# Optimization experiments

Hardware: AMD Instinct MI355X
Metric: run time of the kernel (lower is better)

The kernel has to match this reference:

```python
import jax, jax.numpy as jnp
import numpy as np

B, S, DIM = 1, 2048, 4096
NH, NKV, HD = 32, 8, 128
REPEATS = NH // NKV
ROPE_THETA = 10000.0


def setup_inputs() -> dict:
    key = jax.random.key(0)
    ks = jax.random.split(key, 6)
    x = jax.random.normal(ks[0], (B, S, DIM), jnp.float32) * 0.02
    wq = jax.random.normal(ks[1], (NH * HD, DIM), jnp.float32) * 0.02
    wk = jax.random.normal(ks[2], (NKV * HD, DIM), jnp.float32) * 0.02
    wv = jax.random.normal(ks[3], (NKV * HD, DIM), jnp.float32) * 0.02
    wo = jax.random.normal(ks[4], (DIM, NH * HD), jnp.float32) * 0.02
    # rotary frequencies (real cos/sin form of complex freqs_cis)
    inv_freq = 1.0 / (ROPE_THETA ** (jnp.arange(0, HD, 2, dtype=jnp.float32) / HD))
    ang = jnp.arange(S, dtype=jnp.float32)[:, None] * inv_freq[None, :]  # [S, HD//2]
    freqs_cos = jnp.cos(ang)
    freqs_sin = jnp.sin(ang)
    positions = jnp.arange(S, dtype=jnp.int32)  # prompt phase: all positions
    # additive causal mask
    mask = jnp.where(jnp.tril(jnp.ones((S, S), bool)), 0.0, -1e9).astype(jnp.float32)
    cache_k = jnp.zeros((B, S, NKV, HD), jnp.float32)
    cache_v = jnp.zeros((B, S, NKV, HD), jnp.float32)
    return dict(x=x, wq=wq, wk=wk, wv=wv, wo=wo, freqs_cos=freqs_cos,
                freqs_sin=freqs_sin, cache_k=cache_k, cache_v=cache_v,
                positions=positions, mask=mask)


def apply_rope(t, cos, sin):
    # t: [b, s, h, d]; pairs are (d0,d1),(d2,d3),... matching view_as_complex
    tr = t[..., 0::2]
    ti = t[..., 1::2]
    c = cos[None, :, None, :]
    s = sin[None, :, None, :]
    out_r = tr * c - ti * s
    out_i = tr * s + ti * c
    return jnp.stack([out_r, out_i], axis=-1).reshape(t.shape)


def reference(x, wq, wk, wv, wo, freqs_cos, freqs_sin, cache_k, cache_v, positions, mask):
    b, s, _ = x.shape
    xq = jnp.einsum('bsd,od->bso', x, wq).reshape(b, s, NH, HD)
    xk = jnp.einsum('bsd,od->bso', x, wk).reshape(b, s, NKV, HD)
    xv = jnp.einsum('bsd,od->bso', x, wv).reshape(b, s, NKV, HD)
    xq = apply_rope(xq, freqs_cos, freqs_sin)
    xk = apply_rope(xk, freqs_cos, freqs_sin)
    # KV-cache scatter (prompt phase writes; output uses fresh xk/xv here)
    cache_k = cache_k.at[:, positions].set(xk)
    cache_v = cache_v.at[:, positions].set(xv)
    # GQA: repeat_interleave kv heads to match query heads
    k = jnp.repeat(xk, REPEATS, axis=2).transpose(0, 2, 1, 3)  # [b, NH, s, HD]
    v = jnp.repeat(xv, REPEATS, axis=2).transpose(0, 2, 1, 3)
    q = xq.transpose(0, 2, 1, 3)
    scale = HD ** -0.5
    scores = jnp.einsum('bhqd,bhkd->bhqk', q, k) * scale + mask[None, None]
    probs = jax.nn.softmax(scores.astype(jnp.float32), axis=-1).astype(q.dtype)
    out = jnp.einsum('bhqk,bhkd->bhqd', probs, v)
    out = out.transpose(0, 2, 1, 3).reshape(b, s, NH * HD)
    return jnp.einsum('bso,do->bsd', out, wo)
```

## Files before the change

### kernel.cpp

```cpp
#include <hip/hip_runtime.h>
#include <hip/hip_bf16.h>
#include <stdint.h>

typedef __bf16 bf16_t;
typedef __attribute__((ext_vector_type(8))) __bf16 bf16x8;
typedef __attribute__((ext_vector_type(4))) float f32x4;
typedef __attribute__((ext_vector_type(8))) unsigned short u16x8;

#define S_LEN 2048
#define DIM   4096
#define QKVN  6144
#define NHEAD 32
#define HDIM  128

typedef __attribute__((address_space(1))) unsigned int as1_u32;
typedef __attribute__((address_space(3))) unsigned int as3_u32;

__device__ __forceinline__ unsigned short f2bf(float f) {
  unsigned u = __builtin_bit_cast(unsigned, f);
  u += 0x7fffu + ((u >> 16) & 1u);
  return (unsigned short)(u >> 16);
}

__device__ __forceinline__ void gload_lds16(const void* g, void* l) {
  __builtin_amdgcn_global_load_lds(
      (as1_u32*)(unsigned long long)(uintptr_t)g,
      (as3_u32*)(unsigned int)(uintptr_t)l,
      16, 0, 0);
}

__global__ __launch_bounds__(256) void cvt5_kernel(const float* __restrict__ x,
                                                   const float* __restrict__ wq,
                                                   const float* __restrict__ wk,
                                                   const float* __restrict__ wv,
                                                   const float* __restrict__ wo,
                                                   ushort4* __restrict__ xb,
                                                   ushort4* __restrict__ wqkvb,
                                                   ushort4* __restrict__ wob) {
  const long N0 = 2097152;
  const long N1 = N0 + 4194304;
  const long N2 = N1 + 1048576;
  const long N3 = N2 + 1048576;
  const long N4 = N3 + 4194304;
  long idx = (long)blockIdx.x * 256 + threadIdx.x;
  long stride = (long)gridDim.x * 256;
  for (long i = idx; i < N4; i += stride) {
    const float4* s; ushort4* d; long o;
    if (i < N0)      { s = (const float4*)x;  d = xb;              o = i; }
    else if (i < N1) { s = (const float4*)wq; d = wqkvb;           o = i - N0; }
    else if (i < N2) { s = (const float4*)wk; d = wqkvb + 4194304; o = i - N1; }
    else if (i < N3) { s = (const float4*)wv; d = wqkvb + 5242880; o = i - N2; }
    else             { s = (const float4*)wo; d = wob;             o = i - N3; }
    float4 v = s[o];
    ushort4 r;
    r.x = f2bf(v.x); r.y = f2bf(v.y); r.z = f2bf(v.z); r.w = f2bf(v.w);
    d[o] = r;
  }
}

__device__ __forceinline__ bf16x8 fld(const char* half, int row, int chunk) {
  return *(const bf16x8*)(half + row * 128 + ((chunk ^ (row & 7)) << 4));
}

template <int OUTF32>
__global__ __launch_bounds__(512, 2) void gemm8q(const bf16_t* __restrict__ A,
                                                 const bf16_t* __restrict__ B,
                                                 void* __restrict__ Cout,
                                                 int M, int N, int K, int nxt) {
  __shared__ char lds[147456];
  const int tid = threadIdx.x;
  const int lane = tid & 63, w = tid >> 6;
  const int wm = w >> 2, wn = w & 3;
  const int lg = lane >> 4, lr = lane & 15;
  const int nwg = gridDim.x;
  const int orig = blockIdx.x;
  const int wgid = (orig & 7) * (nwg >> 3) + (orig >> 3);
  const int bx = wgid % nxt, by = wgid / nxt;
  const long rowA = (long)by * 256;
  const long rowB = (long)bx * 192;

  f32x4 acc[8][3];
  const f32x4 z4 = {0.f, 0.f, 0.f, 0.f};
#pragma unroll
  for (int i = 0; i < 8; ++i)
#pragma unroll
    for (int j = 0; j < 3; ++j) acc[i][j] = z4;

  const int r0 = tid >> 3, sl = tid & 7;
  const long xo  = (long)((sl ^ (r0 & 7)) << 3);
  const long aof = (rowA + r0) * (long)K + xo;
  const long bof = (rowB + r0) * (long)K + xo;
  const long j1  = (long)64 * K;
  const long h1  = (long)128 * K;
  const int ld0 = tid * 16, ld1 = (tid + 512) * 16, ld2 = (tid + 1024) * 16;

#define QSTG_A(K0, HALF, BUF3)                                                 \
  { char* hp = lds + (BUF3) * 32768 + (HALF) * 16384;                          \
    gload_lds16(A + aof + (HALF) * h1 + (K0),      hp + ld0);                  \
    gload_lds16(A + aof + (HALF) * h1 + j1 + (K0), hp + ld1); }
#define QSTG_B(K0, DBUF)                                                       \
  { char* bp = lds + 98304 + (DBUF) * 24576;                                   \
    gload_lds16(B + bof + (K0),          bp + ld0);                            \
    gload_lds16(B + bof + j1 + (K0),     bp + ld1);                            \
    gload_lds16(B + bof + 2 * j1 + (K0), bp + ld2); }

  const int nt = K >> 6;
  const int brow = wn * 48;

  QSTG_A(0, 0, 0); QSTG_A(0, 1, 0); QSTG_B(0, 0);
  QSTG_A(64, 0, 1); QSTG_A(64, 1, 1); QSTG_B(64, 1);
  asm volatile("s_waitcnt vmcnt(7)" ::: "memory");
  __builtin_amdgcn_s_barrier();

  bf16x8 af[8][2], bf_[3][2];

  for (int t = 0; t < nt; ++t) {
    const int a3 = t % 3, s3 = (t + 2) % 3, d = t & 1;
    const char* Ah = lds + a3 * 32768 + wm * 16384;
    const char* Br = lds + 98304 + d * 24576;
    const int k2 = (t + 2) << 6;
#pragma unroll
    for (int m = 0; m < 2; ++m) {
      af[m][0] = fld(Ah, m * 16 + lr, lg);
      af[m][1] = fld(Ah, m * 16 + lr, 4 + lg);
    }
#pragma unroll
    for (int n = 0; n < 3; ++n) {
      bf_[n][0] = fld(Br, brow + n * 16 + lr, lg);
      bf_[n][1] = fld(Br, brow + n * 16 + lr, 4 + lg);
    }
    if (t + 2 < nt) QSTG_A(k2, 0, s3);
    __builtin_amdgcn_s_barrier();
    asm volatile("s_waitcnt lgkmcnt(0)" ::: "memory");
    __builtin_amdgcn_sched_barrier(0);
    __builtin_amdgcn_s_setprio(1);
#pragma unroll
    for (int m = 0; m < 2; ++m)
#pragma unroll
      for (int n = 0; n < 3; ++n) {
        acc[m][n] = __builtin_amdgcn_mfma_f32_16x16x32_bf16(af[m][0], bf_[n][0], acc[m][n], 0, 0, 0);
        acc[m][n] = __builtin_amdgcn_mfma_f32_16x16x32_bf16(af[m][1], bf_[n][1], acc[m][n], 0, 0, 0);
      }
    __builtin_amdgcn_s_setprio(0);
    __builtin_amdgcn_s_barrier();
#pragma unroll
    for (int m = 2; m < 4; ++m) {
      af[m][0] = fld(Ah, m * 16 + lr, lg);
      af[m][1] = fld(Ah, m * 16 + lr, 4 + lg);
    }
    if (t + 2 < nt) QSTG_A(k2, 1, s3);
    __builtin_amdgcn_s_barrier();
    asm volatile("s_waitcnt lgkmcnt(0)" ::: "memory");
    __builtin_amdgcn_sched_barrier(0);
    __builtin_amdgcn_s_setprio(1);
#pragma unroll
    for (int m = 2; m < 4; ++m)
#pragma unroll
      for (int n = 0; n < 3; ++n) {
        acc[m][n] = __builtin_amdgcn_mfma_f32_16x16x32_bf16(af[m][0], bf_[n][0], acc[m][n], 0, 0, 0);
        acc[m][n] = __builtin_amdgcn_mfma_f32_16x16x32_bf16(af[m][1], bf_[n][1], acc[m][n], 0, 0, 0);
      }
    __builtin_amdgcn_s_setprio(0);
    __builtin_amdgcn_s_barrier();
#pragma unroll
    for (int m = 4; m < 6; ++m) {
      af[m][0] = fld(Ah, m * 16 + lr, lg);
      af[m][1] = fld(Ah, m * 16 + lr, 4 + lg);
    }
    if (t + 2 < nt) QSTG_B(k2, d);
    __builtin_amdgcn_s_barrier();
    asm volatile("s_waitcnt lgkmcnt(0)" ::: "memory");
    __builtin_amdgcn_sched_barrier(0);
    __builtin_amdgcn_s_setprio(1);
#pragma unroll
    for (int m = 4; m < 6; ++m)
#pragma unroll
      for (int n = 0; n < 3; ++n) {
        acc[m][n] = __builtin_amdgcn_mfma_f32_16x16x32_bf16(af[m][0], bf_[n][0], acc[m][n], 0, 0, 0);
        acc[m][n] = __builtin_amdgcn_mfma_f32_16x16x32_bf16(af[m][1], bf_[n][1], acc[m][n], 0, 0, 0);
      }
    __builtin_amdgcn_s_setprio(0);
    __builtin_amdgcn_s_barrier();
#pragma unroll
    for (int m = 6; m < 8; ++m) {
      af[m][0] = fld(Ah, m * 16 + lr, lg);
      af[m][1] = fld(Ah, m * 16 + lr, 4 + lg);
    }
    __builtin_amdgcn_s_barrier();
    asm volatile("s_waitcnt lgkmcnt(0)" ::: "memory");
    __builtin_amdgcn_sched_barrier(0);
    __builtin_amdgcn_s_setprio(1);
#pragma unroll
    for (int m = 6; m < 8; ++m)
#pragma unroll
      for (int n = 0; n < 3; ++n) {
        acc[m][n] = __builtin_amdgcn_mfma_f32_16x16x32_bf16(af[m][0], bf_[n][0], acc[m][n], 0, 0, 0);
        acc[m][n] = __builtin_amdgcn_mfma_f32_16x16x32_bf16(af[m][1], bf_[n][1], acc[m][n], 0, 0, 0);
      }
    __builtin_amdgcn_s_setprio(0);
    if (t + 2 < nt) {
      asm volatile("s_waitcnt vmcnt(7)" ::: "memory");
    } else {
      asm volatile("s_waitcnt vmcnt(0)" ::: "memory");
    }
    __builtin_amdgcn_s_barrier();
  }
#undef QSTG_A
#undef QSTG_B

  const long crow = rowA + wm * 128;
  const long ccol = rowB + wn * 48;
  unsigned short* C = (unsigned short*)Cout;
#pragma unroll
  for (int mf = 0; mf < 8; ++mf)
#pragma unroll
    for (int j = 0; j < 4; ++j) {
      long row = crow + mf * 16 + lg * 4 + j;
      unsigned short* cp = C + row * N + ccol + lr;
#pragma unroll
      for (int nf = 0; nf < 3; ++nf) cp[nf * 16] = f2bf(acc[mf][nf][j]);
    }
}

template <int OUTF32>
__global__ __launch_bounds__(512, 2) void gemm2p(const bf16_t* __restrict__ A,
                                                 const bf16_t* __restrict__ B,
                                                 void* __restrict__ Cout,
                                                 int M, int N, int K, int nxt) {
  __shared__ char lds[147456];
  const int tid = threadIdx.x;
  const int lane = tid & 63, w = tid >> 6;
  const int wm = w >> 1, wn = w & 1;
  const int lg = lane >> 4, lr = lane & 15;
  const int nwg = gridDim.x;
  const int orig = blockIdx.x;
  const int wgid = (orig & 7) * (nwg >> 3) + (orig >> 3);
  const int bx = wgid % nxt, by = wgid / nxt;
  const long rowA = (long)by * 256;
  const long rowB = (long)bx * 128;

  f32x4 acc[4][4];
  const f32x4 z4 = {0.f, 0.f, 0.f, 0.f};
#pragma unroll
  for (int i = 0; i < 4; ++i)
#pragma unroll
    for (int j = 0; j < 4; ++j) acc[i][j] = z4;

  const int r0 = tid >> 3, sl = tid & 7;
  const long xo  = (long)((sl ^ (r0 & 7)) << 3);
  const long aof = (rowA + r0) * (long)K + xo;
  const long bof = (rowB + r0) * (long)K + xo;
  const long r64 = (long)64 * K;

#define PSTG_A(K0, BUF)                                                        \
  { char* ap = lds + (BUF) * 32768;                                            \
    gload_lds16(A + aof + (K0),           ap + tid * 16);                      \
    gload_lds16(A + aof + r64 + (K0),     ap + (tid + 512) * 16);              \
    gload_lds16(A + aof + 2 * r64 + (K0), ap + (tid + 1024) * 16);             \
    gload_lds16(A + aof + 3 * r64 + (K0), ap + (tid + 1536) * 16); }
#define PSTG_B(K0, BUF)                                                        \
  { char* bp = lds + 98304 + (BUF) * 16384;                                    \
    gload_lds16(B + bof + (K0),       bp + tid * 16);                          \
    gload_lds16(B + bof + r64 + (K0), bp + (tid + 512) * 16); }

  const int nt = K >> 6;

  PSTG_A(0, 0); PSTG_B(0, 0); PSTG_A(64, 1); PSTG_B(64, 1);
  asm volatile("s_waitcnt vmcnt(6)" ::: "memory");
  __builtin_amdgcn_s_barrier();

  bf16x8 af[4][2], bf_[4][2];

  for (int t = 0; t < nt; ++t) {
    const int b3 = t % 3, s3 = (t + 2) % 3;
    const char* Ab = lds + b3 * 32768;
    const char* Bb = lds + 98304 + b3 * 16384;
    const int arow = wm * 64, brow = wn * 64;
    const int k2 = (t + 2) << 6;
#pragma unroll
    for (int m = 0; m < 4; ++m) {
      af[m][0] = fld(Ab, arow + m * 16 + lr, lg);
      af[m][1] = fld(Ab, arow + m * 16 + lr, 4 + lg);
    }
#pragma unroll
    for (int n = 0; n < 2; ++n) {
      bf_[n][0] = fld(Bb, brow + n * 16 + lr, lg);
      bf_[n][1] = fld(Bb, brow + n * 16 + lr, 4 + lg);
    }
    if (t + 2 < nt) PSTG_A(k2, s3);
    __builtin_amdgcn_s_barrier();
    asm volatile("s_waitcnt lgkmcnt(0)" ::: "memory");
    __builtin_amdgcn_sched_barrier(0);
    __builtin_amdgcn_s_setprio(1);
#pragma unroll
    for (int m = 0; m < 4; ++m)
#pragma unroll
      for (int n = 0; n < 2; ++n) {
        acc[m][n] = __builtin_amdgcn_mfma_f32_16x16x32_bf16(af[m][0], bf_[n][0], acc[m][n], 0, 0, 0);
        acc[m][n] = __builtin_amdgcn_mfma_f32_16x16x32_bf16(af[m][1], bf_[n][1], acc[m][n], 0, 0, 0);
      }
    __builtin_amdgcn_s_setprio(0);
    __builtin_amdgcn_s_barrier();
#pragma unroll
    for (int n = 2; n < 4; ++n) {
      bf_[n][0] = fld(Bb, brow + n * 16 + lr, lg);
      bf_[n][1] = fld(Bb, brow + n * 16 + lr, 4 + lg);
    }
    if (t + 2 < nt) PSTG_B(k2, s3);
    __builtin_amdgcn_s_barrier();
    asm volatile("s_waitcnt lgkmcnt(0)" ::: "memory");
    __builtin_amdgcn_sched_barrier(0);
    __builtin_amdgcn_s_setprio(1);
#pragma unroll
    for (int m = 0; m < 4; ++m)
#pragma unroll
      for (int n = 2; n < 4; ++n) {
        acc[m][n] = __builtin_amdgcn_mfma_f32_16x16x32_bf16(af[m][0], bf_[n][0], acc[m][n], 0, 0, 0);
        acc[m][n] = __builtin_amdgcn_mfma_f32_16x16x32_bf16(af[m][1], bf_[n][1], acc[m][n], 0, 0, 0);
      }
    __builtin_amdgcn_s_setprio(0);
    if (t + 2 < nt) {
      asm volatile("s_waitcnt vmcnt(6)" ::: "memory");
    } else {
      asm volatile("s_waitcnt vmcnt(0)" ::: "memory");
    }
    __builtin_amdgcn_s_barrier();
  }
#undef PSTG_A
#undef PSTG_B

  const long crow = rowA + wm * 64;
  const long ccol = rowB + wn * 64;
  if (OUTF32) {
    float* C = (float*)Cout;
#pragma unroll
    for (int mf = 0; mf < 4; ++mf)
#pragma unroll
      for (int j = 0; j < 4; ++j) {
        long row = crow + mf * 16 + lg * 4 + j;
        float* cp = C + row * N + ccol + lr;
#pragma unroll
        for (int nf = 0; nf < 4; ++nf) cp[nf * 16] = acc[mf][nf][j];
      }
  } else {
    unsigned short* C = (unsigned short*)Cout;
#pragma unroll
    for (int mf = 0; mf < 4; ++mf)
#pragma unroll
      for (int j = 0; j < 4; ++j) {
        long row = crow + mf * 16 + lg * 4 + j;
        unsigned short* cp = C + row * N + ccol + lr;
#pragma unroll
        for (int nf = 0; nf < 4; ++nf) cp[nf * 16] = f2bf(acc[mf][nf][j]);
      }
  }
}

__global__ __launch_bounds__(256) void prep_kernel(bf16_t* __restrict__ qkv,
                                                   bf16_t* __restrict__ vT,
                                                   const float* __restrict__ cosb,
                                                   const float* __restrict__ sinb) {
  const int bid = blockIdx.x;
  if (bid < 1024) {
    const int kh = bid & 7;
    const int hd = threadIdx.x & 127;
    const int s0 = (bid >> 3) * 16 + (threadIdx.x >> 7) * 8;
    u16x8 v;
#pragma unroll
    for (int e = 0; e < 8; ++e)
      v[e] = *(const unsigned short*)(qkv + (long)(s0 + e) * QKVN + 5120 + kh * HDIM + hd);
    *(u16x8*)(vT + ((long)kh * HDIM + hd) * S_LEN + s0) = v;
  } else {
    int t = (bid - 1024) * 256 + threadIdx.x;
    int i  = t & 63;
    int sh = t >> 6;
    int hh = sh % 40;
    int s  = sh / 40;
    int col2 = (hh < 32) ? (hh * 64 + i) : (2048 + (hh - 32) * 64 + i);
    unsigned int* p = (unsigned int*)qkv + (long)s * (QKVN / 2) + col2;
    unsigned int v = *p;
    float tr = __builtin_bit_cast(float, (v & 0xffffu) << 16);
    float ti = __builtin_bit_cast(float, v & 0xffff0000u);
    float c  = cosb[s * 64 + i];
    float sn = sinb[s * 64 + i];
    float orr = tr * c - ti * sn;
    float oi  = tr * sn + ti * c;
    *p = (unsigned int)f2bf(orr) | ((unsigned int)f2bf(oi) << 16);
  }
}

__global__ __launch_bounds__(512) void attn_kernel(const bf16_t* __restrict__ qkv,
                                                   const bf16_t* __restrict__ vT,
                                                   unsigned short* __restrict__ ob) {
  __shared__ bf16_t Kt[2][64 * 128];
  __shared__ bf16_t Vt[2][128 * 64];
  __shared__ bf16_t Pl[8 * 16 * 64];
  const int h  = blockIdx.x;
  const int qi = 15 - (int)blockIdx.y;
  const int qb = qi * 128;
  const int kh = h >> 2;
  const int tid = threadIdx.x, lane = tid & 63, w = tid >> 6;
  const int lg = lane >> 4, lr = lane & 15;
  const int qrow0 = qb + w * 16;

  bf16x8 qf[4];
  const bf16_t* qptr = qkv + (long)(qrow0 + lr) * QKVN + h * HDIM + lg * 8;
#pragma unroll
  for (int kk = 0; kk < 4; ++kk) qf[kk] = *(const bf16x8*)(qptr + kk * 32);

  const f32x4 z4 = {0.f, 0.f, 0.f, 0.f};
  f32x4 oacc[8];
#pragma unroll
  for (int c = 0; c < 8; ++c) oacc[c] = z4;
  float m[4]     = {-1e30f, -1e30f, -1e30f, -1e30f};
  float plsum[4] = {0.f, 0.f, 0.f, 0.f};

  char* PlB = (char*)Pl + w * 2048;
  const float SCL2 = 0.08838834764831845f * 1.44269504088896f;
  const int ntiles = 2 * qi + 2;
  const int wqmax = qrow0 + 15;

#define STAGE_KV(T, BUF)                                                       \
  {                                                                            \
    const int kvs = (T) * 64;                                                  \
    _Pragma("unroll")                                                          \
    for (int it = 0; it < 2; ++it) {                                           \
      int cch = tid + it * 512;                                                \
      int r = cch >> 4, c = cch & 15;                                          \
      gload_lds16(qkv + (long)(kvs + r) * QKVN + 4096 + kh * HDIM              \
                      + ((c ^ (r & 7)) * 8),                                   \
                  (char*)Kt[BUF] + cch * 16);                                  \
    }                                                                          \
    _Pragma("unroll")                                                          \
    for (int it = 0; it < 2; ++it) {                                           \
      int cch = tid + it * 512;                                                \
      int hd2 = cch >> 3, c = cch & 7;                                         \
      gload_lds16(vT + ((long)kh * HDIM + hd2) * S_LEN + kvs                   \
                      + ((c ^ (hd2 & 7)) * 8),                                 \
                  (char*)Vt[BUF] + cch * 16);                                  \
    }                                                                          \
  }

  STAGE_KV(0, 0);
  STAGE_KV(1, 1);
  asm volatile("s_waitcnt vmcnt(4)" ::: "memory");
  __builtin_amdgcn_s_barrier();

  for (int t = 0; t < ntiles; ++t) {
    const int kv0 = t * 64;
    const int d = t & 1;
    if (kv0 <= wqmax) {
      char* KtB = (char*)Kt[d];
      char* VtB = (char*)Vt[d];

      f32x4 sf[4];
#pragma unroll
      for (int f = 0; f < 4; ++f) {
        f32x4 a = z4;
        int n = f * 16 + lr;
        int rb = n * 256, sw = (n & 7) << 4;
#pragma unroll
        for (int kk = 0; kk < 4; ++kk) {
          bf16x8 kf = *(const bf16x8*)(KtB + rb + (((kk * 4 + lg) * 16) ^ sw));
          a = __builtin_amdgcn_mfma_f32_16x16x32_bf16(qf[kk], kf, a, 0, 0, 0);
        }
        sf[f] = a;
      }

      float sv[4][4], lmax[4];
      if (kv0 + 63 <= qrow0) {
#pragma unroll
        for (int j = 0; j < 4; ++j) {
#pragma unroll
          for (int f = 0; f < 4; ++f) sv[j][f] = sf[f][j] * SCL2;
          lmax[j] = fmaxf(fmaxf(sv[j][0], sv[j][1]), fmaxf(sv[j][2], sv[j][3]));
        }
      } else {
#pragma unroll
        for (int j = 0; j < 4; ++j) {
          int qrow = qrow0 + lg * 4 + j;
#pragma unroll
          for (int f = 0; f < 4; ++f) {
            float s = sf[f][j] * SCL2;
            if (kv0 + f * 16 + lr > qrow) s = -1e9f;
            sv[j][f] = s;
          }
          lmax[j] = fmaxf(fmaxf(sv[j][0], sv[j][1]), fmaxf(sv[j][2], sv[j][3]));
        }
      }
      float g = fmaxf(fmaxf(lmax[0] - m[0], lmax[1] - m[1]),
                      fmaxf(lmax[2] - m[2], lmax[3] - m[3]));
      if (__any(g > 0.f)) {
#pragma unroll
        for (int j = 0; j < 4; ++j) {
          float t0 = lmax[j];
          t0 = fmaxf(t0, __shfl_xor(t0, 1));
          t0 = fmaxf(t0, __shfl_xor(t0, 2));
          t0 = fmaxf(t0, __shfl_xor(t0, 4));
          t0 = fmaxf(t0, __shfl_xor(t0, 8));
          float mn = fmaxf(m[j], t0);
          float sc;
          asm("v_exp_f32 %0, %1" : "=v"(sc) : "v"(m[j] - mn));
          plsum[j] *= sc;
          m[j] = mn;
#pragma unroll
          for (int c = 0; c < 8; ++c) oacc[c][j] *= sc;
        }
      }
#pragma unroll
      for (int j = 0; j < 4; ++j) {
        float p[4];
#pragma unroll
        for (int f = 0; f < 4; ++f)
          asm("v_exp_f32 %0, %1" : "=v"(p[f]) : "v"(sv[j][f] - m[j]));
        plsum[j] += (p[0] + p[1]) + (p[2] + p[3]);
        int row = lg * 4 + j;
        int swp = (row & 7) << 4;
#pragma unroll
        for (int f = 0; f < 4; ++f)
          *(unsigned short*)(PlB + row * 128 + (((f * 16 + lr) * 2) ^ swp)) = f2bf(p[f]);
      }

      bf16x8 pfr[2];
#pragma unroll
      for (int kk = 0; kk < 2; ++kk)
        pfr[kk] = *(const bf16x8*)(PlB + lr * 128 + (((kk * 4 + lg) * 16) ^ ((lr & 7) << 4)));
#pragma unroll
      for (int c = 0; c < 8; ++c) {
        int hd = c * 16 + lr;
        int rb = hd * 128, sw = (hd & 7) << 4;
#pragma unroll
        for (int kk = 0; kk < 2; ++kk) {
          bf16x8 vf = *(const bf16x8*)(VtB + rb + (((kk * 4 + lg) * 16) ^ sw));
          oacc[c] = __builtin_amdgcn_mfma_f32_16x16x32_bf16(pfr[kk], vf, oacc[c], 0, 0, 0);
        }
      }
    }
    __builtin_amdgcn_s_barrier();
    if (t + 2 < ntiles) {
      STAGE_KV(t + 2, d);
      asm volatile("s_waitcnt vmcnt(4)" ::: "memory");
    } else {
      asm volatile("s_waitcnt vmcnt(0)" ::: "memory");
    }
    __builtin_amdgcn_s_barrier();
  }
#undef STAGE_KV

  float rl[4];
#pragma unroll
  for (int j = 0; j < 4; ++j) {
    float s = plsum[j];
    s += __shfl_xor(s, 1);
    s += __shfl_xor(s, 2);
    s += __shfl_xor(s, 4);
    s += __shfl_xor(s, 8);
    rl[j] = 1.f / s;
  }
#pragma unroll
  for (int c = 0; c < 8; ++c)
#pragma unroll
    for (int j = 0; j < 4; ++j) {
      long row = qrow0 + lg * 4 + j;
      ob[row * 4096 + h * 128 + c * 16 + lr] = f2bf(oacc[c][j] * rl[j]);
    }
}

extern "C" void kernel_launch(void* const* d_in, const int* in_sizes, int n_in,
                              void* d_out, int out_size, void* d_ws, size_t ws_size,
                              hipStream_t stream) {
  const float* x  = (const float*)d_in[0];
  const float* wq = (const float*)d_in[1];
  const float* wk = (const float*)d_in[2];
  const float* wv = (const float*)d_in[3];
  const float* wo = (const float*)d_in[4];
  const float* fc = (const float*)d_in[5];
  const float* fs = (const float*)d_in[6];

  char* ws = (char*)d_ws;
  bf16_t* xb    = (bf16_t*)(ws + 0);
  bf16_t* wqkvb = (bf16_t*)(ws + 16777216);
  bf16_t* wob   = (bf16_t*)(ws + 67108864);
  bf16_t* qkv   = (bf16_t*)(ws + 100663296);
  bf16_t* ob    = (bf16_t*)(ws + 125829120);
  bf16_t* vT    = (bf16_t*)(ws + 0);

  cvt5_kernel<<<2048, 256, 0, stream>>>(x, wq, wk, wv, wo,
                                        (ushort4*)xb, (ushort4*)wqkvb, (ushort4*)wob);

  gemm8q<0><<<256, 512, 0, stream>>>(xb, wqkvb, qkv, 2048, 6144, 4096, 32);
  prep_kernel<<<21504, 256, 0, stream>>>(qkv, vT, fc, fs);
  attn_kernel<<<dim3(32, 16), 512, 0, stream>>>(qkv, vT, (unsigned short*)ob);
  gemm2p<1><<<256, 512, 0, stream>>>(ob, wob, d_out, 2048, 4096, 4096, 32);
}
```

Baseline: 310.7 us.

## Fuse fp32-to-bf16 weight conversion into GEMM B-operand loading

The separate conversion pass over wq/wk/wv/wo is removed. Each GEMM now loads fp32 weight tiles into registers, packs them to bf16 with v_cvt_pk_bf16_f32, and writes them into swizzled LDS. This avoids writing and re-reading a bf16 weight copy in global memory (about 80 MB of fp32 read plus bf16 traffic). In exchange, each weight tile is read as fp32 by every row-block workgroup, which doubles the B-operand global bytes, and the loads go through registers instead of direct-to-LDS. The pipeline waits and barriers are restructured to match, and B staging drops from triple to double buffering in gemm2p.

```diff
diff --git a/kernel.cpp b/kernel.cpp
--- a/kernel.cpp
+++ b/kernel.cpp
@@ -6,6 +6,7 @@
 typedef __attribute__((ext_vector_type(8))) __bf16 bf16x8;
 typedef __attribute__((ext_vector_type(4))) float f32x4;
 typedef __attribute__((ext_vector_type(8))) unsigned short u16x8;
+typedef __attribute__((ext_vector_type(4))) unsigned int u32x4;
 
 #define S_LEN 2048
 #define DIM   4096
@@ -29,32 +30,26 @@
       16, 0, 0);
 }
 
-__global__ __launch_bounds__(256) void cvt5_kernel(const float* __restrict__ x,
-                                                   const float* __restrict__ wq,
-                                                   const float* __restrict__ wk,
-                                                   const float* __restrict__ wv,
-                                                   const float* __restrict__ wo,
-                                                   ushort4* __restrict__ xb,
-                                                   ushort4* __restrict__ wqkvb,
-                                                   ushort4* __restrict__ wob) {
+__device__ __forceinline__ u32x4 cvt8(const float4& lo, const float4& hi) {
+  unsigned q0, q1, q2, q3;
+  asm("v_cvt_pk_bf16_f32 %0, %1, %2" : "=v"(q0) : "v"(lo.x), "v"(lo.y));
+  asm("v_cvt_pk_bf16_f32 %0, %1, %2" : "=v"(q1) : "v"(lo.z), "v"(lo.w));
+  asm("v_cvt_pk_bf16_f32 %0, %1, %2" : "=v"(q2) : "v"(hi.x), "v"(hi.y));
+  asm("v_cvt_pk_bf16_f32 %0, %1, %2" : "=v"(q3) : "v"(hi.z), "v"(hi.w));
+  u32x4 r = {q0, q1, q2, q3};
+  return r;
+}
+
+__global__ __launch_bounds__(256) void cvt_x(const float* __restrict__ x,
+                                             ushort4* __restrict__ xb) {
   const long N0 = 2097152;
-  const long N1 = N0 + 4194304;
-  const long N2 = N1 + 1048576;
-  const long N3 = N2 + 1048576;
-  const long N4 = N3 + 4194304;
   long idx = (long)blockIdx.x * 256 + threadIdx.x;
   long stride = (long)gridDim.x * 256;
-  for (long i = idx; i < N4; i += stride) {
-    const float4* s; ushort4* d; long o;
-    if (i < N0)      { s = (const float4*)x;  d = xb;              o = i; }
-    else if (i < N1) { s = (const float4*)wq; d = wqkvb;           o = i - N0; }
-    else if (i < N2) { s = (const float4*)wk; d = wqkvb + 4194304; o = i - N1; }
-    else if (i < N3) { s = (const float4*)wv; d = wqkvb + 5242880; o = i - N2; }
-    else             { s = (const float4*)wo; d = wob;             o = i - N3; }
-    float4 v = s[o];
+  for (long i = idx; i < N0; i += stride) {
+    float4 v = ((const float4*)x)[i];
     ushort4 r;
     r.x = f2bf(v.x); r.y = f2bf(v.y); r.z = f2bf(v.z); r.w = f2bf(v.w);
-    d[o] = r;
+    xb[i] = r;
   }
 }
 
@@ -62,10 +57,11 @@
   return *(const bf16x8*)(half + row * 128 + ((chunk ^ (row & 7)) << 4));
 }
 
-template <int OUTF32>
 __global__ __launch_bounds__(512, 2) void gemm8q(const bf16_t* __restrict__ A,
-                                                 const bf16_t* __restrict__ B,
-                                                 void* __restrict__ Cout,
+                                                 const float* __restrict__ Wq,
+                                                 const float* __restrict__ Wk,
+                                                 const float* __restrict__ Wv,
+                                                 unsigned short* __restrict__ C,
                                                  int M, int N, int K, int nxt) {
   __shared__ char lds[147456];
   const int tid = threadIdx.x;
@@ -89,35 +85,58 @@
   const int r0 = tid >> 3, sl = tid & 7;
   const long xo  = (long)((sl ^ (r0 & 7)) << 3);
   const long aof = (rowA + r0) * (long)K + xo;
-  const long bof = (rowB + r0) * (long)K + xo;
   const long j1  = (long)64 * K;
   const long h1  = (long)128 * K;
-  const int ld0 = tid * 16, ld1 = (tid + 512) * 16, ld2 = (tid + 1024) * 16;
+  const int ld0 = tid * 16, ld1 = (tid + 512) * 16;
+
+  const float* bsrc[3];
+  int ldsw[3];
+#pragma unroll
+  for (int i = 0; i < 3; ++i) {
+    int c = tid + i * 512;
+    int row = c >> 3, s = c & 7;
+    long grow = rowB + row;
+    const float* base = (grow < 4096) ? (Wq + grow * (long)K)
+                       : (grow < 5120) ? (Wk + (grow - 4096) * (long)K)
+                                       : (Wv + (grow - 5120) * (long)K);
+    bsrc[i] = base + s * 8;
+    ldsw[i] = row * 128 + ((s ^ (row & 7)) << 4);
+  }
 
 #define QSTG_A(K0, HALF, BUF3)                                                 \
   { char* hp = lds + (BUF3) * 32768 + (HALF) * 16384;                          \
     gload_lds16(A + aof + (HALF) * h1 + (K0),      hp + ld0);                  \
     gload_lds16(A + aof + (HALF) * h1 + j1 + (K0), hp + ld1); }
-#define QSTG_B(K0, DBUF)                                                       \
-  { char* bp = lds + 98304 + (DBUF) * 24576;                                   \
-    gload_lds16(B + bof + (K0),          bp + ld0);                            \
-    gload_lds16(B + bof + j1 + (K0),     bp + ld1);                            \
-    gload_lds16(B + bof + 2 * j1 + (K0), bp + ld2); }
+#define QLOAD_B(K0)                                                            \
+  _Pragma("unroll")                                                            \
+  for (int i = 0; i < 3; ++i) {                                                \
+    blo[i] = *(const float4*)(bsrc[i] + (K0));                                 \
+    bhi[i] = *(const float4*)(bsrc[i] + (K0) + 4);                             \
+  }
+#define QWRITE_B(DB)                                                           \
+  { char* bw = lds + 98304 + (DB) * 24576;                                     \
+    _Pragma("unroll")                                                          \
+    for (int i = 0; i < 3; ++i) *(u32x4*)(bw + ldsw[i]) = cvt8(blo[i], bhi[i]); }
 
   const int nt = K >> 6;
   const int brow = wn * 48;
-
-  QSTG_A(0, 0, 0); QSTG_A(0, 1, 0); QSTG_B(0, 0);
-  QSTG_A(64, 0, 1); QSTG_A(64, 1, 1); QSTG_B(64, 1);
-  asm volatile("s_waitcnt vmcnt(7)" ::: "memory");
+  float4 blo[3], bhi[3];
+
+  QSTG_A(0, 0, 0); QSTG_A(0, 1, 0);
+  QSTG_A(64, 0, 1); QSTG_A(64, 1, 1);
+  QLOAD_B(0);
+  asm volatile("s_waitcnt vmcnt(0)" ::: "memory");
+  QWRITE_B(0);
+  QLOAD_B(64);
+  asm volatile("s_waitcnt lgkmcnt(0)" ::: "memory");
   __builtin_amdgcn_s_barrier();
 
   bf16x8 af[8][2], bf_[3][2];
 
   for (int t = 0; t < nt; ++t) {
-    const int a3 = t % 3, s3 = (t + 2) % 3, d = t & 1;
+    const int a3 = t % 3, s3 = (t + 2) % 3;
     const char* Ah = lds + a3 * 32768 + wm * 16384;
-    const char* Br = lds + 98304 + d * 24576;
+    const char* Br = lds + 98304 + (t & 1) * 24576;
     const int k2 = (t + 2) << 6;
 #pragma unroll
     for (int m = 0; m < 2; ++m) {
@@ -167,13 +186,36 @@
       af[m][0] = fld(Ah, m * 16 + lr, lg);
       af[m][1] = fld(Ah, m * 16 + lr, 4 + lg);
     }
-    if (t + 2 < nt) QSTG_B(k2, d);
+    if (t + 1 < nt) {
+      if (t + 2 < nt) { asm volatile("s_waitcnt vmcnt(4)" ::: "memory"); }
+      else            { asm volatile("s_waitcnt vmcnt(0)" ::: "memory"); }
+      QWRITE_B((t + 1) & 1);
+    }
+    if (t + 2 < nt) QLOAD_B(k2);
+    asm volatile("s_waitcnt lgkmcnt(0)" ::: "memory");
+    __builtin_amdgcn_sched_barrier(0);
+    __builtin_amdgcn_s_barrier();
+    __builtin_amdgcn_s_setprio(1);
+#pragma unroll
+    for (int m = 4; m < 6; ++m)
+#pragma unroll
+      for (int n = 0; n < 3; ++n) {
+        acc[m][n] = __builtin_amdgcn_mfma_f32_16x16x32_bf16(af[m][0], bf_[n][0], acc[m][n], 0, 0, 0);
+        acc[m][n] = __builtin_amdgcn_mfma_f32_16x16x32_bf16(af[m][1], bf_[n][1], acc[m][n], 0, 0, 0);
+      }
+    __builtin_amdgcn_s_setprio(0);
+    __builtin_amdgcn_s_barrier();
+#pragma unroll
+    for (int m = 6; m < 8; ++m) {
+      af[m][0] = fld(Ah, m * 16 + lr, lg);
+      af[m][1] = fld(Ah, m * 16 + lr, 4 + lg);
+    }
     __builtin_amdgcn_s_barrier();
     asm volatile("s_waitcnt lgkmcnt(0)" ::: "memory");
     __builtin_amdgcn_sched_barrier(0);
     __builtin_amdgcn_s_setprio(1);
 #pragma unroll
-    for (int m = 4; m < 6; ++m)
+    for (int m = 6; m < 8; ++m)
 #pragma unroll
       for (int n = 0; n < 3; ++n) {
         acc[m][n] = __builtin_amdgcn_mfma_f32_16x16x32_bf16(af[m][0], bf_[n][0], acc[m][n], 0, 0, 0);
@@ -181,36 +223,13 @@
       }
     __builtin_amdgcn_s_setprio(0);
     __builtin_amdgcn_s_barrier();
-#pragma unroll
-    for (int m = 6; m < 8; ++m) {
-      af[m][0] = fld(Ah, m * 16 + lr, lg);
-      af[m][1] = fld(Ah, m * 16 + lr, 4 + lg);
-    }
-    __builtin_amdgcn_s_barrier();
-    asm volatile("s_waitcnt lgkmcnt(0)" ::: "memory");
-    __builtin_amdgcn_sched_barrier(0);
-    __builtin_amdgcn_s_setprio(1);
-#pragma unroll
-    for (int m = 6; m < 8; ++m)
-#pragma unroll
-      for (int n = 0; n < 3; ++n) {
-        acc[m][n] = __builtin_amdgcn_mfma_f32_16x16x32_bf16(af[m][0], bf_[n][0], acc[m][n], 0, 0, 0);
-        acc[m][n] = __builtin_amdgcn_mfma_f32_16x16x32_bf16(af[m][1], bf_[n][1], acc[m][n], 0, 0, 0);
-      }
-    __builtin_amdgcn_s_setprio(0);
-    if (t + 2 < nt) {
-      asm volatile("s_waitcnt vmcnt(7)" ::: "memory");
-    } else {
-      asm volatile("s_waitcnt vmcnt(0)" ::: "memory");
-    }
-    __builtin_amdgcn_s_barrier();
   }
 #undef QSTG_A
-#undef QSTG_B
+#undef QLOAD_B
+#undef QWRITE_B
 
   const long crow = rowA + wm * 128;
   const long ccol = rowB + wn * 48;
-  unsigned short* C = (unsigned short*)Cout;
 #pragma unroll
   for (int mf = 0; mf < 8; ++mf)
 #pragma unroll
@@ -222,12 +241,11 @@
     }
 }
 
-template <int OUTF32>
 __global__ __launch_bounds__(512, 2) void gemm2p(const bf16_t* __restrict__ A,
-                                                 const bf16_t* __restrict__ B,
-                                                 void* __restrict__ Cout,
+                                                 const float* __restrict__ W,
+                                                 float* __restrict__ C,
                                                  int M, int N, int K, int nxt) {
-  __shared__ char lds[147456];
+  __shared__ char lds[131072];
   const int tid = threadIdx.x;
   const int lane = tid & 63, w = tid >> 6;
   const int wm = w >> 1, wn = w & 1;
@@ -249,8 +267,17 @@
   const int r0 = tid >> 3, sl = tid & 7;
   const long xo  = (long)((sl ^ (r0 & 7)) << 3);
   const long aof = (rowA + r0) * (long)K + xo;
-  const long bof = (rowB + r0) * (long)K + xo;
   const long r64 = (long)64 * K;
+
+  const float* bsrc[2];
+  int ldsw[2];
+#pragma unroll
+  for (int i = 0; i < 2; ++i) {
+    int c = tid + i * 512;
+    int row = c >> 3, s = c & 7;
+    bsrc[i] = W + (rowB + row) * (long)K + s * 8;
+    ldsw[i] = row * 128 + ((s ^ (row & 7)) << 4);
+  }
 
 #define PSTG_A(K0, BUF)                                                        \
   { char* ap = lds + (BUF) * 32768;                                            \
@@ -258,15 +285,26 @@
     gload_lds16(A + aof + r64 + (K0),     ap + (tid + 512) * 16);              \
     gload_lds16(A + aof + 2 * r64 + (K0), ap + (tid + 1024) * 16);             \
     gload_lds16(A + aof + 3 * r64 + (K0), ap + (tid + 1536) * 16); }
-#define PSTG_B(K0, BUF)                                                        \
-  { char* bp = lds + 98304 + (BUF) * 16384;                                    \
-    gload_lds16(B + bof + (K0),       bp + tid * 16);                          \
-    gload_lds16(B + bof + r64 + (K0), bp + (tid + 512) * 16); }
+#define PLOAD_B(K0)                                                            \
+  _Pragma("unroll")                                                            \
+  for (int i = 0; i < 2; ++i) {                                                \
+    blo[i] = *(const float4*)(bsrc[i] + (K0));                                 \
+    bhi[i] = *(const float4*)(bsrc[i] + (K0) + 4);                             \
+  }
+#define PWRITE_B(DB)                                                           \
+  { char* bw = lds + 98304 + (DB) * 16384;                                     \
+    _Pragma("unroll")                                                          \
+    for (int i = 0; i < 2; ++i) *(u32x4*)(bw + ldsw[i]) = cvt8(blo[i], bhi[i]); }
 
   const int nt = K >> 6;
-
-  PSTG_A(0, 0); PSTG_B(0, 0); PSTG_A(64, 1); PSTG_B(64, 1);
-  asm volatile("s_waitcnt vmcnt(6)" ::: "memory");
+  float4 blo[2], bhi[2];
+
+  PSTG_A(0, 0); PSTG_A(64, 1);
+  PLOAD_B(0);
+  asm volatile("s_waitcnt vmcnt(0)" ::: "memory");
+  PWRITE_B(0);
+  PLOAD_B(64);
+  asm volatile("s_waitcnt lgkmcnt(0)" ::: "memory");
   __builtin_amdgcn_s_barrier();
 
   bf16x8 af[4][2], bf_[4][2];
@@ -274,7 +312,7 @@
   for (int t = 0; t < nt; ++t) {
     const int b3 = t % 3, s3 = (t + 2) % 3;
     const char* Ab = lds + b3 * 32768;
-    const char* Bb = lds + 98304 + b3 * 16384;
+    const char* Bb = lds + 98304 + (t & 1) * 16384;
     const int arow = wm * 64, brow = wn * 64;
     const int k2 = (t + 2) << 6;
 #pragma unroll
@@ -306,10 +344,15 @@
       bf_[n][0] = fld(Bb, brow + n * 16 + lr, lg);
       bf_[n][1] = fld(Bb, brow + n * 16 + lr, 4 + lg);
     }
-    if (t + 2 < nt) PSTG_B(k2, s3);
-    __builtin_amdgcn_s_barrier();
+    if (t + 1 < nt) {
+      if (t + 2 < nt) { asm volatile("s_waitcnt vmcnt(4)" ::: "memory"); }
+      else            { asm volatile("s_waitcnt vmcnt(0)" ::: "memory"); }
+      PWRITE_B((t + 1) & 1);
+    }
+    if (t + 2 < nt) PLOAD_B(k2);
     asm volatile("s_waitcnt lgkmcnt(0)" ::: "memory");
     __builtin_amdgcn_sched_barrier(0);
+    __builtin_amdgcn_s_barrier();
     __builtin_amdgcn_s_setprio(1);
 #pragma unroll
     for (int m = 0; m < 4; ++m)
@@ -319,41 +362,23 @@
         acc[m][n] = __builtin_amdgcn_mfma_f32_16x16x32_bf16(af[m][1], bf_[n][1], acc[m][n], 0, 0, 0);
       }
     __builtin_amdgcn_s_setprio(0);
-    if (t + 2 < nt) {
-      asm volatile("s_waitcnt vmcnt(6)" ::: "memory");
-    } else {
-      asm volatile("s_waitcnt vmcnt(0)" ::: "memory");
-    }
     __builtin_amdgcn_s_barrier();
   }
 #undef PSTG_A
-#undef PSTG_B
+#undef PLOAD_B
+#undef PWRITE_B
 
   const long crow = rowA + wm * 64;
   const long ccol = rowB + wn * 64;
-  if (OUTF32) {
-    float* C = (float*)Cout;
-#pragma unroll
-    for (int mf = 0; mf < 4; ++mf)
-#pragma unroll
-      for (int j = 0; j < 4; ++j) {
-        long row = crow + mf * 16 + lg * 4 + j;
-        float* cp = C + row * N + ccol + lr;
-#pragma unroll
-        for (int nf = 0; nf < 4; ++nf) cp[nf * 16] = acc[mf][nf][j];
-      }
-  } else {
-    unsigned short* C = (unsigned short*)Cout;
-#pragma unroll
-    for (int mf = 0; mf < 4; ++mf)
-#pragma unroll
-      for (int j = 0; j < 4; ++j) {
-        long row = crow + mf * 16 + lg * 4 + j;
-        unsigned short* cp = C + row * N + ccol + lr;
-#pragma unroll
-        for (int nf = 0; nf < 4; ++nf) cp[nf * 16] = f2bf(acc[mf][nf][j]);
-      }
-  }
+#pragma unroll
+  for (int mf = 0; mf < 4; ++mf)
+#pragma unroll
+    for (int j = 0; j < 4; ++j) {
+      long row = crow + mf * 16 + lg * 4 + j;
+      float* cp = C + row * N + ccol + lr;
+#pragma unroll
+      for (int nf = 0; nf < 4; ++nf) cp[nf * 16] = acc[mf][nf][j];
+    }
 }
 
 __global__ __launch_bounds__(256) void prep_kernel(bf16_t* __restrict__ qkv,
@@ -578,18 +603,16 @@
   const float* fs = (const float*)d_in[6];
 
   char* ws = (char*)d_ws;
-  bf16_t* xb    = (bf16_t*)(ws + 0);
-  bf16_t* wqkvb = (bf16_t*)(ws + 16777216);
-  bf16_t* wob   = (bf16_t*)(ws + 67108864);
-  bf16_t* qkv   = (bf16_t*)(ws + 100663296);
-  bf16_t* ob    = (bf16_t*)(ws + 125829120);
-  bf16_t* vT    = (bf16_t*)(ws + 0);
-
-  cvt5_kernel<<<2048, 256, 0, stream>>>(x, wq, wk, wv, wo,
-                                        (ushort4*)xb, (ushort4*)wqkvb, (ushort4*)wob);
-
-  gemm8q<0><<<256, 512, 0, stream>>>(xb, wqkvb, qkv, 2048, 6144, 4096, 32);
+  bf16_t* xb  = (bf16_t*)(ws + 0);
+  bf16_t* qkv = (bf16_t*)(ws + 100663296);
+  bf16_t* ob  = (bf16_t*)(ws + 125829120);
+  bf16_t* vT  = (bf16_t*)(ws + 33554432);
+
+  cvt_x<<<1024, 256, 0, stream>>>(x, (ushort4*)xb);
+
+  gemm8q<<<256, 512, 0, stream>>>(xb, wq, wk, wv, (unsigned short*)qkv,
+                                  2048, 6144, 4096, 32);
   prep_kernel<<<21504, 256, 0, stream>>>(qkv, vT, fc, fs);
   attn_kernel<<<dim3(32, 16), 512, 0, stream>>>(qkv, vT, (unsigned short*)ob);
-  gemm2p<1><<<256, 512, 0, stream>>>(ob, wob, d_out, 2048, 4096, 4096, 32);
-}
+  gemm2p<<<256, 512, 0, stream>>>(ob, wo, (float*)d_out, 2048, 4096, 4096, 32);
+}
```

After: 331.9 us. +6.8%, slower.
